# Optimization experiments

Hardware: AMD Instinct MI355X
Metric: run time of the kernel (lower is better)

The kernel has to match this reference:

```python
import jax, jax.numpy as jnp
import numpy as np

B, N, D, H, E = 4, 2048, 512, 8, 64  # batch, seq, model dim, heads, head dim
EPS = 1e-6
PAD = -2.0
NEG_INF = -1000000000.0
ROPE_MAX = 2048
ROPE_BASE = 10000.0


def compute_rope_rotations(dim, max_seq_len, base):
    inv_freq = 1.0 / base ** (jnp.arange(0, dim, 2, dtype=jnp.float32) / dim)
    pos = jnp.arange(max_seq_len, dtype=jnp.float32)
    freqs = pos[:, None] * inv_freq[None, :]          # (L, dim/2)
    freqs = jnp.repeat(freqs, 2, axis=-1)             # (L, dim)
    return jnp.cos(freqs), jnp.sin(freqs)


def apply_rope(x, cos, sin):
    # Faithful to the source: positions are indexed along AXIS 1 of x.
    # Since q/k have layout (b, h, n, e), axis 1 is the HEAD axis (source quirk).
    seq = x.shape[1]
    c = cos[:seq][None, :, None, :]
    s = sin[:seq][None, :, None, :]
    x1, x2 = x[..., 0::2], x[..., 1::2]
    ch, sh = c[..., 0::2], s[..., 0::2]
    r1 = x1 * ch - x2 * sh
    r2 = x1 * sh + x2 * ch
    return jnp.stack([r1, r2], axis=-1).reshape(x.shape)


def layer_norm(x, gamma, beta):
    mean = jnp.mean(x, axis=-1, keepdims=True)
    var = jnp.mean(jnp.square(x - mean), axis=-1, keepdims=True)
    return gamma * ((x - mean) / jnp.sqrt(var + EPS)) + beta


def setup_inputs() -> dict:
    key = jax.random.key(0)
    ks = jax.random.split(key, 10)
    x = jax.random.normal(ks[0], (B, N, D), dtype=jnp.float32)
    mask = jnp.where(jax.random.uniform(ks[1], (B, N)) < 0.1, PAD, 1.0).astype(jnp.float32)
    glorot_qkv = float(np.sqrt(6.0 / (D + E)))
    q_proj = jax.random.uniform(ks[2], (H, D, E), minval=-glorot_qkv, maxval=glorot_qkv, dtype=jnp.float32)
    k_proj = jax.random.uniform(ks[3], (H, D, E), minval=-glorot_qkv, maxval=glorot_qkv, dtype=jnp.float32)
    v_proj = jax.random.uniform(ks[4], (H, D, E), minval=-glorot_qkv, maxval=glorot_qkv, dtype=jnp.float32)
    g = jax.random.uniform(ks[5], (H, D, E), minval=-0.05, maxval=0.05, dtype=jnp.float32)
    glorot_out = float(np.sqrt(6.0 / (H * E + D)))
    out_w = jax.random.uniform(ks[6], (H * E, D), minval=-glorot_out, maxval=glorot_out, dtype=jnp.float32)
    out_b = jnp.zeros((D,), dtype=jnp.float32)
    gamma_in = jnp.ones((D,), dtype=jnp.float32)
    beta_in = jnp.zeros((D,), dtype=jnp.float32)
    gamma_out = jnp.ones((D,), dtype=jnp.float32)
    beta_out = jnp.zeros((D,), dtype=jnp.float32)
    rope_cos, rope_sin = compute_rope_rotations(E, ROPE_MAX, ROPE_BASE)
    return dict(x=x, mask=mask, q_proj=q_proj, k_proj=k_proj, v_proj=v_proj, g=g,
                gamma_in=gamma_in, beta_in=beta_in, gamma_out=gamma_out, beta_out=beta_out,
                out_w=out_w, out_b=out_b, rope_cos=rope_cos, rope_sin=rope_sin)


def reference(x, mask, q_proj, k_proj, v_proj, g, gamma_in, beta_in,
              gamma_out, beta_out, out_w, out_b, rope_cos, rope_sin):
    scale = 1.0 / jnp.sqrt(jnp.asarray(E, dtype=x.dtype))
    q_input = layer_norm(x, gamma_in, beta_in)          # self-attention: shared LN input
    mask_bin = jnp.where(mask == PAD, 0.0, 1.0).astype(x.dtype)  # (B, N)
    q = jnp.einsum('bnd,hde->bhne', q_input, q_proj)
    k = jnp.einsum('bmd,hde->bhme', q_input, k_proj)
    v = jnp.einsum('bmd,hde->bhme', q_input, v_proj)
    q = apply_rope(q, rope_cos, rope_sin)
    k = apply_rope(k, rope_cos, rope_sin)
    att = jnp.einsum('bhne,bhme->bhnm', q, k) * scale   # (B, H, N, N)
    amask = mask_bin[:, None, :, None] * mask_bin[:, None, None, :]  # (B,1,N,N)
    att = att + (1.0 - amask) * NEG_INF
    att = jax.nn.softmax(att, axis=-1) * amask
    out = jnp.einsum('bhnm,bhme->bhne', att, v)
    gate = jax.nn.sigmoid(jnp.einsum('bnd,hde->bhne', q_input, g))
    out = out * gate
    out = out.transpose(0, 2, 1, 3).reshape(x.shape[0], x.shape[1], H * E)
    out = out @ out_w + out_b
    out = out + x  # residual
    return layer_norm(out, gamma_out, beta_out)


if __name__ == '__main__':
    inp = setup_inputs()
    y = reference(**inp)
    print(y.shape, y.dtype)
```

## Files before the change

### kernel.cpp

```cpp
#include <hip/hip_runtime.h>
#include <math.h>

#define B_ 4
#define N_ 2048
#define D_ 512
#define H_ 8
#define E_ 64

constexpr float EPS = 1e-6f;
constexpr float PADV = -2.0f;
constexpr float SCL = 0.18033688011112043f;

typedef __attribute__((ext_vector_type(8))) __bf16 bf16x8;
typedef __attribute__((ext_vector_type(4))) float f32x4;
typedef __attribute__((ext_vector_type(8))) unsigned short u16x8;

__device__ inline unsigned short f2bf(float f) {
  unsigned u = __builtin_bit_cast(unsigned, f);
  u += 0x7fffu + ((u >> 16) & 1u);
  return (unsigned short)(u >> 16);
}
__device__ inline float bf2f(unsigned short v) {
  unsigned u = ((unsigned)v) << 16;
  return __builtin_bit_cast(float, u);
}

__global__ __launch_bounds__(256) void prep_kernel(
    const float* __restrict__ qp, const float* __restrict__ kp,
    const float* __restrict__ vp, const float* __restrict__ gp,
    const float* __restrict__ ow, ushort* __restrict__ wT,
    ushort* __restrict__ owT) {
  __shared__ float Ls[64][65];
  int t = threadIdx.x;
  const float* src;
  ushort* dst;
  int src_ld, r0, c0;
  if (blockIdx.x < 256) {
    int set = blockIdx.x >> 6, tile = blockIdx.x & 63;
    int h = tile >> 3, dt = tile & 7;
    const float* w = set == 0 ? qp : set == 1 ? kp : set == 2 ? vp : gp;
    src = w + (size_t)h * 512 * 64;
    src_ld = 64;
    r0 = dt * 64;
    c0 = 0;
    dst = wT + ((size_t)set * 512 + h * 64) * 512;
  } else {
    int idx = blockIdx.x - 256;
    src = ow;
    src_ld = 512;
    r0 = (idx >> 3) * 64;
    c0 = (idx & 7) * 64;
    dst = owT;
  }
#pragma unroll
  for (int i = 0; i < 4; i++) {
    int id = t + i * 256;
    int r = id >> 4, c4 = (id & 15) * 4;
    float4 v = *(const float4*)(src + (size_t)(r0 + r) * src_ld + c0 + c4);
    Ls[r][c4] = v.x;
    Ls[r][c4 + 1] = v.y;
    Ls[r][c4 + 2] = v.z;
    Ls[r][c4 + 3] = v.w;
  }
  __syncthreads();
#pragma unroll
  for (int i = 0; i < 4; i++) {
    int id = t + i * 256;
    int c = id >> 4, r4 = (id & 15) * 4;
    ushort4 o;
    o.x = f2bf(Ls[r4][c]);
    o.y = f2bf(Ls[r4 + 1][c]);
    o.z = f2bf(Ls[r4 + 2][c]);
    o.w = f2bf(Ls[r4 + 3][c]);
    *(ushort4*)(dst + (size_t)(c0 + c) * 512 + r0 + r4) = o;
  }
}

__global__ __launch_bounds__(256) void ln_bf16_kernel(
    const float* __restrict__ x, const float* __restrict__ gamma,
    const float* __restrict__ beta, ushort* __restrict__ out) {
  int row = blockIdx.x;
  const float* xr = x + (size_t)row * D_;
  int c0 = threadIdx.x, c1 = threadIdx.x + 256;
  float v0 = xr[c0], v1 = xr[c1];
  __shared__ float red[8];
  int lane = threadIdx.x & 63, wid = threadIdx.x >> 6;
  float s = v0 + v1;
  for (int o = 32; o > 0; o >>= 1) s += __shfl_down(s, o, 64);
  if (lane == 0) red[wid] = s;
  __syncthreads();
  float mean = (red[0] + red[1] + red[2] + red[3]) * (1.0f / D_);
  float d0 = v0 - mean, d1 = v1 - mean;
  float sq = d0 * d0 + d1 * d1;
  for (int o = 32; o > 0; o >>= 1) sq += __shfl_down(sq, o, 64);
  if (lane == 0) red[4 + wid] = sq;
  __syncthreads();
  float var = (red[4] + red[5] + red[6] + red[7]) * (1.0f / D_);
  float rstd = rsqrtf(var + EPS);
  ushort* orow = out + (size_t)row * D_;
  orow[c0] = f2bf(gamma[c0] * (d0 * rstd) + beta[c0]);
  orow[c1] = f2bf(gamma[c1] * (d1 * rstd) + beta[c1]);
}

__global__ __launch_bounds__(256) void ln_kernel(
    const float* __restrict__ x, const float* __restrict__ gamma,
    const float* __restrict__ beta, float* __restrict__ out) {
  int row = blockIdx.x;
  const float* xr = x + (size_t)row * D_;
  int c0 = threadIdx.x, c1 = threadIdx.x + 256;
  float v0 = xr[c0], v1 = xr[c1];
  __shared__ float red[8];
  int lane = threadIdx.x & 63, wid = threadIdx.x >> 6;
  float s = v0 + v1;
  for (int o = 32; o > 0; o >>= 1) s += __shfl_down(s, o, 64);
  if (lane == 0) red[wid] = s;
  __syncthreads();
  float mean = (red[0] + red[1] + red[2] + red[3]) * (1.0f / D_);
  float d0 = v0 - mean, d1 = v1 - mean;
  float sq = d0 * d0 + d1 * d1;
  for (int o = 32; o > 0; o >>= 1) sq += __shfl_down(sq, o, 64);
  if (lane == 0) red[4 + wid] = sq;
  __syncthreads();
  float var = (red[4] + red[5] + red[6] + red[7]) * (1.0f / D_);
  float rstd = rsqrtf(var + EPS);
  float* orow = out + (size_t)row * D_;
  orow[c0] = gamma[c0] * (d0 * rstd) + beta[c0];
  orow[c1] = gamma[c1] * (d1 * rstd) + beta[c1];
}

__global__ __launch_bounds__(256) void proj_kernel(
    const ushort* __restrict__ xbf, const ushort* __restrict__ wT,
    const float* __restrict__ rope_cos, const float* __restrict__ rope_sin,
    ushort* __restrict__ qo, ushort* __restrict__ ko,
    ushort* __restrict__ vTo, ushort* __restrict__ go) {
  int tileM = blockIdx.x;
  int h = blockIdx.y & 7;
  int set = blockIdx.y >> 3;

  __shared__ ushort As[128 * 64];
  __shared__ ushort Bs[64 * 64];

  const int t = threadIdx.x;
  const int w = t >> 6;
  const int lane = t & 63;
  const int quad = lane >> 4;
  const int n15 = lane & 15;

  const ushort* wbase = wT + ((size_t)set * 512 + h * 64) * 512;
  const int bn0 = tileM * 128;

  f32x4 acc[2][4];
#pragma unroll
  for (int mb = 0; mb < 2; mb++)
#pragma unroll
    for (int tt = 0; tt < 4; tt++) acc[mb][tt] = (f32x4){0.f, 0.f, 0.f, 0.f};

  for (int k0 = 0; k0 < 512; k0 += 64) {
    __syncthreads();
#pragma unroll
    for (int i = 0; i < 4; i++) {
      int c = t + i * 256;
      int row = c >> 3, c8 = c & 7;
      *(uint4*)&As[(row << 6) + ((c8 ^ (row & 7)) << 3)] =
          *(const uint4*)(xbf + (size_t)(bn0 + row) * 512 + k0 + (c8 << 3));
    }
#pragma unroll
    for (int i = 0; i < 2; i++) {
      int c = t + i * 256;
      int row = c >> 3, c8 = c & 7;
      *(uint4*)&Bs[(row << 6) + ((c8 ^ (row & 7)) << 3)] =
          *(const uint4*)(wbase + (size_t)row * 512 + k0 + (c8 << 3));
    }
    __syncthreads();
#pragma unroll
    for (int kk = 0; kk < 2; kk++) {
      bf16x8 af[2], bfr[4];
#pragma unroll
      for (int mb = 0; mb < 2; mb++) {
        int m = 32 * w + 16 * mb + n15;
        af[mb] = __builtin_bit_cast(
            bf16x8,
            *(const uint4*)&As[(m << 6) + ((((kk << 2) + quad) ^ (m & 7)) << 3)]);
      }
#pragma unroll
      for (int tt = 0; tt < 4; tt++) {
        int n = 16 * tt + n15;
        bfr[tt] = __builtin_bit_cast(
            bf16x8,
            *(const uint4*)&Bs[(n << 6) + ((((kk << 2) + quad) ^ (n & 7)) << 3)]);
      }
#pragma unroll
      for (int mb = 0; mb < 2; mb++)
#pragma unroll
        for (int tt = 0; tt < 4; tt++)
          acc[mb][tt] = __builtin_amdgcn_mfma_f32_16x16x32_bf16(
              af[mb], bfr[tt], acc[mb][tt], 0, 0, 0);
    }
  }

  const int b = bn0 >> 11;
  const int n_base = bn0 & 2047;
  const int bh = b * H_ + h;
  const size_t bhN = (size_t)bh * N_;

  if (set <= 1) {
    ushort* dst = (set == 0) ? qo : ko;
    const float oscale = (set == 0) ? SCL : 1.0f;
    const float sgn = (n15 & 1) ? 1.f : -1.f;
#pragma unroll
    for (int tt = 0; tt < 4; tt++) {
      int e = 16 * tt + n15;
      float cv = rope_cos[(h << 6) + e];
      float sv = rope_sin[(h << 6) + e];
#pragma unroll
      for (int mb = 0; mb < 2; mb++) {
#pragma unroll
        for (int r = 0; r < 4; r++) {
          float xv = acc[mb][tt][r];
          float pv = __shfl_xor(xv, 1, 64);
          float ov = (xv * cv + sgn * pv * sv) * oscale;
          int n = n_base + 32 * w + 16 * mb + 4 * quad + r;
          dst[((bhN + n) << 6) + e] = f2bf(ov);
        }
      }
    }
  } else if (set == 2) {
#pragma unroll
    for (int tt = 0; tt < 4; tt++) {
      int e = 16 * tt + n15;
#pragma unroll
      for (int mb = 0; mb < 2; mb++) {
        int n0 = n_base + 32 * w + 16 * mb + 4 * quad;
        ushort4 pk;
        pk.x = f2bf(acc[mb][tt][0]);
        pk.y = f2bf(acc[mb][tt][1]);
        pk.z = f2bf(acc[mb][tt][2]);
        pk.w = f2bf(acc[mb][tt][3]);
        *(ushort4*)(vTo + ((size_t)(bh * 64 + e)) * N_ + n0) = pk;
      }
    }
  } else {
#pragma unroll
    for (int tt = 0; tt < 4; tt++) {
      int e = 16 * tt + n15;
#pragma unroll
      for (int mb = 0; mb < 2; mb++) {
#pragma unroll
        for (int r = 0; r < 4; r++) {
          int n = n_base + 32 * w + 16 * mb + 4 * quad + r;
          float sv = 1.0f / (1.0f + __expf(-acc[mb][tt][r]));
          go[((bhN + n) << 6) + e] = f2bf(sv);
        }
      }
    }
  }
}

__global__ __launch_bounds__(512, 4) void attn_kernel(
    const ushort* __restrict__ qb, const ushort* __restrict__ kb,
    const ushort* __restrict__ vT, const ushort* __restrict__ gb,
    const float* __restrict__ mask, ushort* __restrict__ out) {
  int qt = blockIdx.x;
  int bh = blockIdx.y;
  int b = bh >> 3, h = bh & 7;

  __shared__ __align__(16) uint arena[12928];

  const int t = threadIdx.x;
  const int w = t >> 6;
  const int grp = w >> 2;
  const int gw = w & 3;
  const int lane = t & 63;
  const int quad = lane >> 4;
  const int n15 = lane & 15;
  const int sw = n15 & 7;
  const int tg = t & 255;

  uint* Ks = &arena[grp * 4096];
  uint* Vts = &arena[grp * 4096 + 2048];
  uint* Pq = &arena[8192 + w * 576];
  float* kmbf = (float*)&arena[12800];

  const size_t bhN = (size_t)bh * N_;
  const size_t bN = (size_t)b * N_;
  const int q0 = qt * 128 + 32 * gw;
  const int koff = grp << 10;

  bf16x8 qf[2][2];
#pragma unroll
  for (int mb = 0; mb < 2; mb++) {
    const ushort* qrow = qb + ((bhN + q0 + 16 * mb + n15) << 6);
#pragma unroll
    for (int hf = 0; hf < 2; hf++)
      qf[mb][hf] = __builtin_bit_cast(
          bf16x8, *(const uint4*)(qrow + 32 * hf + (quad << 3)));
  }

  bf16x8 ones;
  {
    u16x8 ou;
#pragma unroll
    for (int j = 0; j < 8; j++) ou[j] = 0x3F80;
    ones = __builtin_bit_cast(bf16x8, ou);
  }

  f32x4 O[2][4], O5[2];
#pragma unroll
  for (int mb = 0; mb < 2; mb++) {
    O5[mb] = (f32x4){0.f, 0.f, 0.f, 0.f};
#pragma unroll
    for (int tt = 0; tt < 4; tt++) O[mb][tt] = (f32x4){0.f, 0.f, 0.f, 0.f};
  }

  for (int it = 0; it < 16; it++) {
    int m0 = koff + (it << 6);
    __syncthreads();
#pragma unroll
    for (int i = 0; i < 2; i++) {
      int idx = tg + (i << 8);
      int row = idx >> 3, c8 = idx & 7;
      int dst = row * 32 + ((c8 ^ (row & 7)) << 2);
      *(uint4*)&Ks[dst] =
          *(const uint4*)(kb + ((bhN + m0 + row) << 6) + (c8 << 3));
      *(uint4*)&Vts[dst] =
          *(const uint4*)(vT + (size_t)(bh * 64 + row) * N_ + m0 + (c8 << 3));
    }
    if (tg < 16) {
      f32x4 mv = *(const f32x4*)(mask + bN + m0 + 4 * tg);
      f32x4 bias;
#pragma unroll
      for (int j = 0; j < 4; j++) bias[j] = (mv[j] == PADV) ? -1e9f : 0.f;
      *(f32x4*)&kmbf[(grp << 6) + 4 * tg] = bias;
    }
    __syncthreads();

    f32x4 bias[4];
#pragma unroll
    for (int tt = 0; tt < 4; tt++)
      bias[tt] = *(const f32x4*)&kmbf[(grp << 6) + 16 * tt + 4 * quad];

    f32x4 st[2][4];
#pragma unroll
    for (int mb = 0; mb < 2; mb++)
#pragma unroll
      for (int tt = 0; tt < 4; tt++) st[mb][tt] = bias[tt];
#pragma unroll
    for (int hf = 0; hf < 2; hf++) {
#pragma unroll
      for (int tt = 0; tt < 4; tt++) {
        bf16x8 kf = __builtin_bit_cast(
            bf16x8, *(const uint4*)&Ks[(16 * tt + n15) * 32 +
                                       (((quad + 4 * hf) ^ sw) << 2)]);
        st[0][tt] = __builtin_amdgcn_mfma_f32_16x16x32_bf16(kf, qf[0][hf],
                                                            st[0][tt], 0, 0, 0);
        st[1][tt] = __builtin_amdgcn_mfma_f32_16x16x32_bf16(kf, qf[1][hf],
                                                            st[1][tt], 0, 0, 0);
      }
    }

    bf16x8 pf[2][2];
#pragma unroll
    for (int mb = 0; mb < 2; mb++) {
      int rowb = n15 * 36;
#pragma unroll
      for (int tt = 0; tt < 4; tt++) {
        uint u0 = __builtin_bit_cast(
                      uint, __builtin_exp2f(fminf(st[mb][tt][0], 60.f))) +
                  0x8000u;
        uint u1 = __builtin_bit_cast(
                      uint, __builtin_exp2f(fminf(st[mb][tt][1], 60.f))) +
                  0x8000u;
        uint u2 = __builtin_bit_cast(
                      uint, __builtin_exp2f(fminf(st[mb][tt][2], 60.f))) +
                  0x8000u;
        uint u3 = __builtin_bit_cast(
                      uint, __builtin_exp2f(fminf(st[mb][tt][3], 60.f))) +
                  0x8000u;
        int a = rowb + ((2 * tt + (quad >> 1)) << 2) + ((quad & 1) << 1);
        Pq[a] = __builtin_amdgcn_perm(u1, u0, 0x07060302u);
        Pq[a + 1] = __builtin_amdgcn_perm(u3, u2, 0x07060302u);
      }
      __asm__ volatile("" ::: "memory");
#pragma unroll
      for (int hf = 0; hf < 2; hf++)
        pf[mb][hf] = __builtin_bit_cast(
            bf16x8, *(const uint4*)&Pq[n15 * 36 + ((quad + 4 * hf) << 2)]);
      __asm__ volatile("" ::: "memory");
    }

#pragma unroll
    for (int hf = 0; hf < 2; hf++) {
      O5[0] = __builtin_amdgcn_mfma_f32_16x16x32_bf16(pf[0][hf], ones, O5[0],
                                                      0, 0, 0);
      O5[1] = __builtin_amdgcn_mfma_f32_16x16x32_bf16(pf[1][hf], ones, O5[1],
                                                      0, 0, 0);
#pragma unroll
      for (int tt = 0; tt < 4; tt++) {
        bf16x8 vf = __builtin_bit_cast(
            bf16x8, *(const uint4*)&Vts[(16 * tt + n15) * 32 +
                                        (((quad + 4 * hf) ^ sw) << 2)]);
        O[0][tt] = __builtin_amdgcn_mfma_f32_16x16x32_bf16(pf[0][hf], vf,
                                                           O[0][tt], 0, 0, 0);
        O[1][tt] = __builtin_amdgcn_mfma_f32_16x16x32_bf16(pf[1][hf], vf,
                                                           O[1][tt], 0, 0, 0);
      }
    }
  }

  __syncthreads();
  f32x4* cbuf = (f32x4*)arena;
  int ci = (gw * 64 + lane) * 10;
  if (grp == 1) {
#pragma unroll
    for (int mb = 0; mb < 2; mb++)
#pragma unroll
      for (int tt = 0; tt < 4; tt++) cbuf[ci + mb * 4 + tt] = O[mb][tt];
    cbuf[ci + 8] = O5[0];
    cbuf[ci + 9] = O5[1];
  }
  __syncthreads();
  if (grp == 0) {
#pragma unroll
    for (int mb = 0; mb < 2; mb++)
#pragma unroll
      for (int tt = 0; tt < 4; tt++) O[mb][tt] += cbuf[ci + mb * 4 + tt];
    O5[0] += cbuf[ci + 8];
    O5[1] += cbuf[ci + 9];

#pragma unroll
    for (int mb = 0; mb < 2; mb++) {
#pragma unroll
      for (int r = 0; r < 4; r++) {
        int n = q0 + 16 * mb + 4 * quad + r;
        float qm = (mask[bN + n] == PADV) ? 0.f : 1.f;
        float inv = qm / fmaxf(O5[mb][r], 1e-30f);
        const ushort* grow = gb + ((bhN + n) << 6);
        ushort* orow = out + ((bN + n) << 9) + (h << 6);
#pragma unroll
        for (int tt = 0; tt < 4; tt++) {
          int e = 16 * tt + n15;
          orow[e] = f2bf(O[mb][tt][r] * inv * bf2f(grow[e]));
        }
      }
    }
  }
}

__global__ __launch_bounds__(256) void outproj_kernel(
    const ushort* __restrict__ ain, const ushort* __restrict__ owT,
    const float* __restrict__ bias, const float* __restrict__ xres,
    float* __restrict__ out) {
  int tileM = blockIdx.x;
  int cc0 = blockIdx.y * 64;

  __shared__ ushort As[128 * 64];
  __shared__ ushort Bs[64 * 64];

  const int t = threadIdx.x;
  const int w = t >> 6;
  const int lane = t & 63;
  const int quad = lane >> 4;
  const int n15 = lane & 15;

  const ushort* wbase = owT + (size_t)cc0 * 512;
  const int bn0 = tileM * 128;

  f32x4 acc[2][4];
#pragma unroll
  for (int mb = 0; mb < 2; mb++)
#pragma unroll
    for (int tt = 0; tt < 4; tt++) acc[mb][tt] = (f32x4){0.f, 0.f, 0.f, 0.f};

  for (int k0 = 0; k0 < 512; k0 += 64) {
    __syncthreads();
#pragma unroll
    for (int i = 0; i < 4; i++) {
      int c = t + i * 256;
      int row = c >> 3, c8 = c & 7;
      *(uint4*)&As[(row << 6) + ((c8 ^ (row & 7)) << 3)] =
          *(const uint4*)(ain + (size_t)(bn0 + row) * 512 + k0 + (c8 << 3));
    }
#pragma unroll
    for (int i = 0; i < 2; i++) {
      int c = t + i * 256;
      int row = c >> 3, c8 = c & 7;
      *(uint4*)&Bs[(row << 6) + ((c8 ^ (row & 7)) << 3)] =
          *(const uint4*)(wbase + (size_t)row * 512 + k0 + (c8 << 3));
    }
    __syncthreads();
#pragma unroll
    for (int kk = 0; kk < 2; kk++) {
      bf16x8 af[2], bfr[4];
#pragma unroll
      for (int mb = 0; mb < 2; mb++) {
        int m = 32 * w + 16 * mb + n15;
        af[mb] = __builtin_bit_cast(
            bf16x8,
            *(const uint4*)&As[(m << 6) + ((((kk << 2) + quad) ^ (m & 7)) << 3)]);
      }
#pragma unroll
      for (int tt = 0; tt < 4; tt++) {
        int n = 16 * tt + n15;
        bfr[tt] = __builtin_bit_cast(
            bf16x8,
            *(const uint4*)&Bs[(n << 6) + ((((kk << 2) + quad) ^ (n & 7)) << 3)]);
      }
#pragma unroll
      for (int mb = 0; mb < 2; mb++)
#pragma unroll
        for (int tt = 0; tt < 4; tt++)
          acc[mb][tt] = __builtin_amdgcn_mfma_f32_16x16x32_bf16(
              af[mb], bfr[tt], acc[mb][tt], 0, 0, 0);
    }
  }

#pragma unroll
  for (int tt = 0; tt < 4; tt++) {
    int c = cc0 + 16 * tt + n15;
    float bv = bias[c];
#pragma unroll
    for (int mb = 0; mb < 2; mb++) {
#pragma unroll
      for (int r = 0; r < 4; r++) {
        size_t row = bn0 + 32 * w + 16 * mb + 4 * quad + r;
        out[row * 512 + c] = acc[mb][tt][r] + bv + xres[row * 512 + c];
      }
    }
  }
}

extern "C" void kernel_launch(void* const* d_in, const int* in_sizes, int n_in,
                              void* d_out, int out_size, void* d_ws,
                              size_t ws_size, hipStream_t stream) {
  (void)in_sizes; (void)n_in; (void)out_size; (void)ws_size;
  const float* x = (const float*)d_in[0];
  const float* mask = (const float*)d_in[1];
  const float* q_proj = (const float*)d_in[2];
  const float* k_proj = (const float*)d_in[3];
  const float* v_proj = (const float*)d_in[4];
  const float* g = (const float*)d_in[5];
  const float* gamma_in = (const float*)d_in[6];
  const float* beta_in = (const float*)d_in[7];
  const float* gamma_out = (const float*)d_in[8];
  const float* beta_out = (const float*)d_in[9];
  const float* out_w = (const float*)d_in[10];
  const float* out_b = (const float*)d_in[11];
  const float* rope_cos = (const float*)d_in[12];
  const float* rope_sin = (const float*)d_in[13];

  char* p = (char*)d_ws;
  ushort* xbf   = (ushort*)p; p += (size_t)8 << 20;
  ushort* wT    = (ushort*)p; p += (size_t)2 << 20;
  ushort* owT   = (ushort*)p; p += (size_t)1 << 20;
  ushort* qb16  = (ushort*)p; p += (size_t)8 << 20;
  ushort* kb16  = (ushort*)p; p += (size_t)8 << 20;
  ushort* vT16  = (ushort*)p; p += (size_t)8 << 20;
  ushort* gate  = (ushort*)p; p += (size_t)8 << 20;
  ushort* attnb = (ushort*)p; p += (size_t)8 << 20;
  float* ypre   = (float*)p;  p += (size_t)16 << 20;

  prep_kernel<<<320, 256, 0, stream>>>(q_proj, k_proj, v_proj, g, out_w, wT,
                                       owT);

  ln_bf16_kernel<<<B_ * N_, 256, 0, stream>>>(x, gamma_in, beta_in, xbf);

  dim3 gp(64, 32);
  proj_kernel<<<gp, 256, 0, stream>>>(xbf, wT, rope_cos, rope_sin, qb16, kb16,
                                      vT16, gate);

  dim3 ga(16, 32);
  attn_kernel<<<ga, 512, 0, stream>>>(qb16, kb16, vT16, gate, mask, attnb);

  dim3 go(64, 8);
  outproj_kernel<<<go, 256, 0, stream>>>(attnb, owT, out_b, x, ypre);

  ln_kernel<<<B_ * N_, 256, 0, stream>>>(ypre, gamma_out, beta_out,
                                         (float*)d_out);
}
```

Baseline: 223.8 us.

## Drop split-K across wave groups in attention, use 256-thread blocks

The attention kernel no longer splits the key range between two 4-wave groups and merges their partial sums through shared memory. Each 256-thread block now walks all 2048 keys itself, which removes the final reduction and its barriers. Each wave also gets separate P buffers per m-block, so the exp/pack writes for both blocks can happen before any reads. The cost is half as many waves per block, a serial loop twice as long per block, and possibly lower latency hiding.

```diff
diff --git a/kernel.cpp b/kernel.cpp
--- a/kernel.cpp
+++ b/kernel.cpp
@@ -256,7 +256,7 @@
   }
 }
 
-__global__ __launch_bounds__(512, 4) void attn_kernel(
+__global__ __launch_bounds__(256) void attn_kernel(
     const ushort* __restrict__ qb, const ushort* __restrict__ kb,
     const ushort* __restrict__ vT, const ushort* __restrict__ gb,
     const float* __restrict__ mask, ushort* __restrict__ out) {
@@ -264,27 +264,21 @@
   int bh = blockIdx.y;
   int b = bh >> 3, h = bh & 7;
 
-  __shared__ __align__(16) uint arena[12928];
+  __shared__ uint Ksu[64 * 32];
+  __shared__ uint Vtsu[64 * 32];
+  __shared__ uint Pw[4 * 2 * 576];
+  __shared__ __align__(16) float kmb[64];
 
   const int t = threadIdx.x;
   const int w = t >> 6;
-  const int grp = w >> 2;
-  const int gw = w & 3;
   const int lane = t & 63;
   const int quad = lane >> 4;
   const int n15 = lane & 15;
   const int sw = n15 & 7;
-  const int tg = t & 255;
-
-  uint* Ks = &arena[grp * 4096];
-  uint* Vts = &arena[grp * 4096 + 2048];
-  uint* Pq = &arena[8192 + w * 576];
-  float* kmbf = (float*)&arena[12800];
 
   const size_t bhN = (size_t)bh * N_;
   const size_t bN = (size_t)b * N_;
-  const int q0 = qt * 128 + 32 * gw;
-  const int koff = grp << 10;
+  const int q0 = qt * 128 + 32 * w;
 
   bf16x8 qf[2][2];
 #pragma unroll
@@ -312,45 +306,43 @@
     for (int tt = 0; tt < 4; tt++) O[mb][tt] = (f32x4){0.f, 0.f, 0.f, 0.f};
   }
 
-  for (int it = 0; it < 16; it++) {
-    int m0 = koff + (it << 6);
+  uint* Pq[2] = {&Pw[(w * 2) * 576], &Pw[(w * 2 + 1) * 576]};
+
+  for (int m0 = 0; m0 < N_; m0 += 64) {
     __syncthreads();
 #pragma unroll
     for (int i = 0; i < 2; i++) {
-      int idx = tg + (i << 8);
+      int idx = t + (i << 8);
       int row = idx >> 3, c8 = idx & 7;
       int dst = row * 32 + ((c8 ^ (row & 7)) << 2);
-      *(uint4*)&Ks[dst] =
+      *(uint4*)&Ksu[dst] =
           *(const uint4*)(kb + ((bhN + m0 + row) << 6) + (c8 << 3));
-      *(uint4*)&Vts[dst] =
+      *(uint4*)&Vtsu[dst] =
           *(const uint4*)(vT + (size_t)(bh * 64 + row) * N_ + m0 + (c8 << 3));
     }
-    if (tg < 16) {
-      f32x4 mv = *(const f32x4*)(mask + bN + m0 + 4 * tg);
+    if (t < 16) {
+      f32x4 mv = *(const f32x4*)(mask + bN + m0 + 4 * t);
       f32x4 bias;
 #pragma unroll
       for (int j = 0; j < 4; j++) bias[j] = (mv[j] == PADV) ? -1e9f : 0.f;
-      *(f32x4*)&kmbf[(grp << 6) + 4 * tg] = bias;
+      *(f32x4*)&kmb[4 * t] = bias;
     }
     __syncthreads();
 
-    f32x4 bias[4];
-#pragma unroll
-    for (int tt = 0; tt < 4; tt++)
-      bias[tt] = *(const f32x4*)&kmbf[(grp << 6) + 16 * tt + 4 * quad];
-
     f32x4 st[2][4];
 #pragma unroll
-    for (int mb = 0; mb < 2; mb++)
-#pragma unroll
-      for (int tt = 0; tt < 4; tt++) st[mb][tt] = bias[tt];
+    for (int tt = 0; tt < 4; tt++) {
+      f32x4 bias = *(const f32x4*)&kmb[16 * tt + 4 * quad];
+      st[0][tt] = bias;
+      st[1][tt] = bias;
+    }
 #pragma unroll
     for (int hf = 0; hf < 2; hf++) {
 #pragma unroll
       for (int tt = 0; tt < 4; tt++) {
         bf16x8 kf = __builtin_bit_cast(
-            bf16x8, *(const uint4*)&Ks[(16 * tt + n15) * 32 +
-                                       (((quad + 4 * hf) ^ sw) << 2)]);
+            bf16x8, *(const uint4*)&Ksu[(16 * tt + n15) * 32 +
+                                        (((quad + 4 * hf) ^ sw) << 2)]);
         st[0][tt] = __builtin_amdgcn_mfma_f32_16x16x32_bf16(kf, qf[0][hf],
                                                             st[0][tt], 0, 0, 0);
         st[1][tt] = __builtin_amdgcn_mfma_f32_16x16x32_bf16(kf, qf[1][hf],
@@ -358,9 +350,9 @@
       }
     }
 
-    bf16x8 pf[2][2];
 #pragma unroll
     for (int mb = 0; mb < 2; mb++) {
+      uint* P = Pq[mb];
       int rowb = n15 * 36;
 #pragma unroll
       for (int tt = 0; tt < 4; tt++) {
@@ -377,16 +369,20 @@
                       uint, __builtin_exp2f(fminf(st[mb][tt][3], 60.f))) +
                   0x8000u;
         int a = rowb + ((2 * tt + (quad >> 1)) << 2) + ((quad & 1) << 1);
-        Pq[a] = __builtin_amdgcn_perm(u1, u0, 0x07060302u);
-        Pq[a + 1] = __builtin_amdgcn_perm(u3, u2, 0x07060302u);
-      }
-      __asm__ volatile("" ::: "memory");
+        P[a] = __builtin_amdgcn_perm(u1, u0, 0x07060302u);
+        P[a + 1] = __builtin_amdgcn_perm(u3, u2, 0x07060302u);
+      }
+    }
+    __asm__ volatile("" ::: "memory");
+
+    bf16x8 pf[2][2];
+#pragma unroll
+    for (int mb = 0; mb < 2; mb++)
 #pragma unroll
       for (int hf = 0; hf < 2; hf++)
         pf[mb][hf] = __builtin_bit_cast(
-            bf16x8, *(const uint4*)&Pq[n15 * 36 + ((quad + 4 * hf) << 2)]);
-      __asm__ volatile("" ::: "memory");
-    }
+            bf16x8,
+            *(const uint4*)&Pq[mb][n15 * 36 + ((quad + 4 * hf) << 2)]);
 
 #pragma unroll
     for (int hf = 0; hf < 2; hf++) {
@@ -397,8 +393,8 @@
 #pragma unroll
       for (int tt = 0; tt < 4; tt++) {
         bf16x8 vf = __builtin_bit_cast(
-            bf16x8, *(const uint4*)&Vts[(16 * tt + n15) * 32 +
-                                        (((quad + 4 * hf) ^ sw) << 2)]);
+            bf16x8, *(const uint4*)&Vtsu[(16 * tt + n15) * 32 +
+                                         (((quad + 4 * hf) ^ sw) << 2)]);
         O[0][tt] = __builtin_amdgcn_mfma_f32_16x16x32_bf16(pf[0][hf], vf,
                                                            O[0][tt], 0, 0, 0);
         O[1][tt] = __builtin_amdgcn_mfma_f32_16x16x32_bf16(pf[1][hf], vf,
@@ -407,40 +403,19 @@
     }
   }
 
-  __syncthreads();
-  f32x4* cbuf = (f32x4*)arena;
-  int ci = (gw * 64 + lane) * 10;
-  if (grp == 1) {
-#pragma unroll
-    for (int mb = 0; mb < 2; mb++)
-#pragma unroll
-      for (int tt = 0; tt < 4; tt++) cbuf[ci + mb * 4 + tt] = O[mb][tt];
-    cbuf[ci + 8] = O5[0];
-    cbuf[ci + 9] = O5[1];
-  }
-  __syncthreads();
-  if (grp == 0) {
-#pragma unroll
-    for (int mb = 0; mb < 2; mb++)
-#pragma unroll
-      for (int tt = 0; tt < 4; tt++) O[mb][tt] += cbuf[ci + mb * 4 + tt];
-    O5[0] += cbuf[ci + 8];
-    O5[1] += cbuf[ci + 9];
-
-#pragma unroll
-    for (int mb = 0; mb < 2; mb++) {
-#pragma unroll
-      for (int r = 0; r < 4; r++) {
-        int n = q0 + 16 * mb + 4 * quad + r;
-        float qm = (mask[bN + n] == PADV) ? 0.f : 1.f;
-        float inv = qm / fmaxf(O5[mb][r], 1e-30f);
-        const ushort* grow = gb + ((bhN + n) << 6);
-        ushort* orow = out + ((bN + n) << 9) + (h << 6);
-#pragma unroll
-        for (int tt = 0; tt < 4; tt++) {
-          int e = 16 * tt + n15;
-          orow[e] = f2bf(O[mb][tt][r] * inv * bf2f(grow[e]));
-        }
+#pragma unroll
+  for (int mb = 0; mb < 2; mb++) {
+#pragma unroll
+    for (int r = 0; r < 4; r++) {
+      int n = q0 + 16 * mb + 4 * quad + r;
+      float qm = (mask[bN + n] == PADV) ? 0.f : 1.f;
+      float inv = qm / fmaxf(O5[mb][r], 1e-30f);
+      const ushort* grow = gb + ((bhN + n) << 6);
+      ushort* orow = out + ((bN + n) << 9) + (h << 6);
+#pragma unroll
+      for (int tt = 0; tt < 4; tt++) {
+        int e = tt * 16 + n15;
+        orow[e] = f2bf(O[mb][tt][r] * inv * bf2f(grow[e]));
       }
     }
   }
@@ -569,7 +544,7 @@
                                       vT16, gate);
 
   dim3 ga(16, 32);
-  attn_kernel<<<ga, 512, 0, stream>>>(qb16, kb16, vT16, gate, mask, attnb);
+  attn_kernel<<<ga, 256, 0, stream>>>(qb16, kb16, vT16, gate, mask, attnb);
 
   dim3 go(64, 8);
   outproj_kernel<<<go, 256, 0, stream>>>(attnb, owT, out_b, x, ypre);
```

After: 225.5 us. Within noise of the previous version (+0.7%).
